# Kernel optimization log

Hardware: AMD Instinct MI355X
Metric: run time of the kernel (lower is better)

## Reference

```python
import jax, jax.numpy as jnp
import numpy as np
from jax import lax

V, D, B, L, T, H, C = 100000, 128, 512, 20, 20, 32, 33
N, E = B * L, B * (L - 1)
SCALE = 12.0

def _l2n(x, eps=1e-12):
    return x / (jnp.linalg.norm(x, axis=-1, keepdims=True) + eps)

def setup_inputs():
    key = jax.random.key(0)
    ks = jax.random.split(key, 30)
    stdv = 1.0 / np.sqrt(D)
    u = lambda k, s: jax.random.uniform(k, s, jnp.float32, -stdv, stdv)
    params = dict(
        emb=u(ks[0], (V, D)),
        W1=u(ks[1], (D, D)), W2=u(ks[2], (D, D)),
        gru_wih=u(ks[3], (3 * D, 2 * D)), gru_whh=u(ks[4], (3 * D, D)),
        gru_bih=u(ks[5], (3 * D,)), gru_bhh=u(ks[6], (3 * D,)),
        fcu_w=u(ks[7], (D, D)), fcv_w=u(ks[8], (D, D)), fcv_b=u(ks[9], (D,)),
        fce_w=u(ks[10], (D,)), fcsr_w=u(ks[11], (D, 2 * D)),
        red_w=u(ks[12], (H, D)), red_b=u(ks[13], (H,)),
        rec_w=u(ks[14], (D, H)), rec_b=u(ks[15], (D,)),
        cde_w1=u(ks[16], (128, H)), cde_b1=u(ks[17], (128,)),
        cde_w2=u(ks[18], (C * H, 128)), cde_b2=u(ks[19], (C * H,)),
        init_w=u(ks[20], (H, C)), init_b=u(ks[21], (H,)),
    )
    nodes = jnp.arange(N).reshape(B, L)  # B session graphs, L nodes each
    params.update(
        w=jax.random.uniform(ks[22], (E,), jnp.float32, 0.1, 1.0),
        times=jnp.cumsum(jax.random.uniform(ks[23], (B, T), jnp.float32, 0.05, 1.0), axis=1),
        iid=jax.random.randint(ks[24], (N,), 0, V),
        src=nodes[:, :-1].reshape(-1),
        dst=nodes[:, 1:].reshape(-1),
        seg_ids=jnp.repeat(jnp.arange(B), L),
        last_nodes=nodes[:, -1],
        embeds_ids=jax.random.randint(ks[25], (B, T), 0, V),
    )
    return params

def reference(emb, W1, W2, gru_wih, gru_whh, gru_bih, gru_bhh, fcu_w, fcv_w, fcv_b,
              fce_w, fcsr_w, red_w, red_b, rec_w, rec_b, cde_w1, cde_b1, cde_w2,
              cde_b2, init_w, init_b, w, times, iid, src, dst, seg_ids, last_nodes,
              embeds_ids):
    feat = _l2n(emb[iid])  # [N,D]
    # --- SRGNN layer: edge-weighted mean message passing (both directions) + GRUCell ---
    def wmean(s, d):
        msum = jax.ops.segment_sum(feat[s] * w[:, None], d, num_segments=N)
        wsum = jax.ops.segment_sum(w, d, num_segments=N)[:, None]
        return jnp.where(wsum > 0, msum / jnp.where(wsum == 0, 1.0, wsum), 0.0)
    hn = jnp.concatenate([wmean(src, dst) @ W1.T, wmean(dst, src) @ W2.T], axis=1)
    gi = hn @ gru_wih.T + gru_bih
    gh = feat @ gru_whh.T + gru_bhh
    i_r, i_z, i_n = jnp.split(gi, 3, axis=1)
    h_r, h_z, h_n = jnp.split(gh, 3, axis=1)
    r = jax.nn.sigmoid(i_r + h_r)
    zg = jax.nn.sigmoid(i_z + h_z)
    ng = jnp.tanh(i_n + r * h_n)
    out = (1.0 - zg) * ng + zg * feat  # NOTE: computed but unused downstream, exactly as original
    # --- neural CDE over the session item sequence (linear interp knots at t=0..T-1, RK4 per knot) ---
    fode = _l2n(emb[embeds_ids] @ red_w.T + red_b)          # [B,T,H]
    X = jnp.concatenate([times[..., None], fode], axis=-1)  # [B,T,C]
    z0 = X[:, 0] @ init_w.T + init_b                        # [B,H]
    def fz(zt):
        h1 = jax.nn.relu(zt @ cde_w1.T + cde_b1)
        return jnp.tanh(h1 @ cde_w2.T + cde_b2).reshape(B, H, C)
    dX = jnp.swapaxes(X[:, 1:] - X[:, :-1], 0, 1)           # [T-1,B,C] piecewise-constant dX/dt
    def step(zt, dx):
        g = lambda zz: jnp.einsum('bhc,bc->bh', fz(zz), dx)
        k1 = g(zt); k2 = g(zt + 0.5 * k1); k3 = g(zt + 0.5 * k2); k4 = g(zt + k3)
        return zt + (k1 + 2.0 * k2 + 2.0 * k3 + k4) / 6.0, None
    zT, _ = lax.scan(step, z0, dX)
    time_embeds = zT @ rec_w.T + rec_b                      # [B,D]
    # --- attention readout over graph segments ---
    featn = feat / jnp.linalg.norm(feat, axis=-1, keepdims=True)  # no-eps renorm, as original
    fu = featn @ fcu_w.T
    fv = featn[last_nodes] @ fcv_w.T + fcv_b
    e = jax.nn.sigmoid(fu + fv[seg_ids]) @ fce_w            # [N]
    emax = jax.ops.segment_max(e, seg_ids, num_segments=B)
    ee = jnp.exp(e - emax[seg_ids])
    alpha = ee / jax.ops.segment_sum(ee, seg_ids, num_segments=B)[seg_ids]
    sr_g = jax.ops.segment_sum(featn * alpha[:, None], seg_ids, num_segments=B)
    sr_l = featn[last_nodes]
    sr = _l2n(jnp.concatenate([sr_l, sr_g], axis=1) @ fcsr_w.T + time_embeds)
    logits = sr @ _l2n(emb).T                               # [B,V]
    return jax.nn.log_softmax(SCALE * logits, axis=-1)
```

## Files before the change

### kernel.cpp

```cpp
#include <hip/hip_runtime.h>
#include <cstdint>

#define VN 100000
#define DD 128
#define BB 512
#define LL 20
#define TT 20
#define HH 32
#define CC 33
#define NC (HH*CC)

typedef unsigned int u32;

#define DEV static __device__ __forceinline__

DEV float tanh_fast(float x){ float e=__expf(2.f*x); return 1.f - 2.f/(e+1.f); }

DEV float rdlane(float v, int l){
  return __int_as_float(__builtin_amdgcn_readlane(__float_as_int(v), l));
}

__global__ __launch_bounds__(576) void k_cde(
    const float* __restrict__ emb, const int* __restrict__ eids,
    const float* __restrict__ times,
    const float* __restrict__ red_w, const float* __restrict__ red_b,
    const float* __restrict__ w1, const float* __restrict__ b1,
    const float* __restrict__ w2, const float* __restrict__ b2,
    const float* __restrict__ iw, const float* __restrict__ ib,
    const float* __restrict__ rw, const float* __restrict__ rb,
    float* __restrict__ te){
  __shared__ float s_u[40*DD + 32*129];
  __shared__ float s_X[2*TT*CC];
  __shared__ float s_b1[DD];
  __shared__ float s_h1[2*DD];
  __shared__ float s_z[64], s_zs[64], s_ks[64], s_kp[64], s_kt[64];
  __shared__ float s_dx[2*CC];
  const int t = threadIdx.x;
  const int b0 = blockIdx.x*2;
  const int lane = t & 63;
  float* s_er = s_u;
  float* s_rw = s_u + 40*DD;
  float* s_w1 = s_u;

  float w2a[DD], w2b[DD];
  float b2a, b2b;
  int hq=0, qq=0;
  if (t < 512){
    hq = t>>4; qq = t&15;
    const int n0 = hq*CC + 2*qq;
    const float4* r0=(const float4*)(w2+(size_t)n0*DD);
    const float4* r1=(const float4*)(w2+(size_t)(n0+1)*DD);
    #pragma unroll 32
    for(int j=0;j<32;j++){
      float4 a=r0[j];
      w2a[4*j]=a.x; w2a[4*j+1]=a.y; w2a[4*j+2]=a.z; w2a[4*j+3]=a.w;
    }
    #pragma unroll 32
    for(int j=0;j<32;j++){
      float4 bv=r1[j];
      w2b[4*j]=bv.x; w2b[4*j+1]=bv.y; w2b[4*j+2]=bv.z; w2b[4*j+3]=bv.w;
    }
    b2a=b2[n0]; b2b=b2[n0+1];
  } else {
    const int l=t-512; const int nt=(l&31)*CC+32;
    const float4* r0=(const float4*)(w2+(size_t)nt*DD);
    #pragma unroll 32
    for(int j=0;j<32;j++){
      float4 a=r0[j];
      w2a[4*j]=a.x; w2a[4*j+1]=a.y; w2a[4*j+2]=a.z; w2a[4*j+3]=a.w;
    }
    b2a=b2[nt]; b2b=0.f;
  }

  for (int i=t;i<HH*DD;i+=576){ int hh=i>>7, d=i&127; s_rw[hh*129+d]=red_w[i]; }
  if (t<40){ int g=t/TT, tt2=t%TT; s_X[(g*TT+tt2)*CC]=times[(b0+g)*TT+tt2]; }
  for (int p=t;p<40*DD;p+=576){ int r=p>>7, e=p&127;
      s_er[p]=emb[(size_t)eids[b0*TT + r]*DD + e]; }
  __syncthreads();
  for (int task=t; task<40*HH; task+=576){
    int r=task>>5, hh=task&31;
    const float* wr=s_rw+hh*129;
    const float* er=s_er+(size_t)r*DD;
    float acc=red_b[hh];
    #pragma unroll 16
    for(int e=0;e<DD;e++) acc += er[e]*wr[e];
    float ss=acc*acc;
    #pragma unroll
    for(int o=16;o>0;o>>=1) ss+=__shfl_xor(ss,o,32);
    s_X[r*CC+1+hh]=acc/(sqrtf(ss)+1e-12f);
  }
  __syncthreads();
  for (int i=t;i<DD*HH;i+=576){ int j=i>>5, hh=i&31; s_w1[j*33+hh]=w1[i]; }
  if (t<DD) s_b1[t]=b1[t];
  if (t<64){
    int g=t>>5, hh=t&31;
    float acc=ib[hh];
    const float* x0=s_X+(size_t)(g*TT)*CC;
    #pragma unroll
    for(int c=0;c<CC;c++) acc += x0[c]*iw[hh*CC+c];
    s_z[t]=acc; s_zs[t]=acc;
  }

  for (int step=0; step<TT-1; step++){
    __syncthreads();
    if (t<2*CC){ int g=t/CC, c=t-g*CC;
      s_dx[t]=s_X[(g*TT+step+1)*CC+c]-s_X[(g*TT+step)*CC+c]; }
    __syncthreads();
    float dx00=0.f,dx01=0.f,dx10=0.f,dx11=0.f,dxt=0.f;
    if (t<512){ int c0=2*qq;
      dx00=s_dx[c0]; dx01=s_dx[c0+1]; dx10=s_dx[CC+c0]; dx11=s_dx[CC+c0+1];
    } else { int l=t-512; dxt=s_dx[(l>>5)*CC+32]; }

    for (int s=0;s<4;s++){
      if (t<256){
        const int g=t>>7, j=t&127, gb=(t>>7)*32;
        float zsv=s_zs[lane];
        float acc=s_b1[j];
        const float* wj=s_w1+j*33;
        #pragma unroll 32
        for(int hh=0;hh<32;hh++) acc += rdlane(zsv, gb+hh)*wj[hh];
        s_h1[g*DD+j]=fmaxf(acc,0.f);
      }
      __syncthreads();
      float h00=s_h1[lane],    h01=s_h1[64+lane];
      float h10=s_h1[DD+lane], h11=s_h1[DD+64+lane];
      if (t<512){
        float a00=b2a, a10=b2b, a01=b2a, a11=b2b;
        #pragma unroll 64
        for(int j=0;j<64;j++){
          float s0=rdlane(h00,j), s1=rdlane(h10,j);
          a00+=s0*w2a[j]; a10+=s0*w2b[j];
          a01+=s1*w2a[j]; a11+=s1*w2b[j];
        }
        #pragma unroll 64
        for(int j=0;j<64;j++){
          float s0=rdlane(h01,j), s1=rdlane(h11,j);
          a00+=s0*w2a[64+j]; a10+=s0*w2b[64+j];
          a01+=s1*w2a[64+j]; a11+=s1*w2b[64+j];
        }
        float pk0=tanh_fast(a00)*dx00 + tanh_fast(a10)*dx01;
        float pk1=tanh_fast(a01)*dx10 + tanh_fast(a11)*dx11;
        #pragma unroll
        for(int o=8;o>0;o>>=1){
          pk0+=__shfl_xor(pk0,o,16);
          pk1+=__shfl_xor(pk1,o,16);
        }
        if (qq==0){ s_kp[hq]=pk0; s_kp[32+hq]=pk1; }
      } else {
        const int l=t-512, gq=l>>5, ht=l&31;
        float a0=0.f, a1=0.f;
        #pragma unroll 64
        for(int j=0;j<64;j++){
          a0+=rdlane(h00,j)*w2a[j];
          a1+=rdlane(h10,j)*w2a[j];
        }
        #pragma unroll 64
        for(int j=0;j<64;j++){
          a0+=rdlane(h01,j)*w2a[64+j];
          a1+=rdlane(h11,j)*w2a[64+j];
        }
        float av = b2a + (gq ? a1 : a0);
        s_kt[gq*32+ht]=tanh_fast(av)*dxt;
      }
      __syncthreads();
      if (t<64){
        float k=s_kp[t]+s_kt[t];
        float zv=s_z[t];
        if(s==0){ s_ks[t]=k;        s_zs[t]=zv+0.5f*k; }
        else if(s==1){ s_ks[t]+=2.f*k; s_zs[t]=zv+0.5f*k; }
        else if(s==2){ s_ks[t]+=2.f*k; s_zs[t]=zv+k; }
        else { float zn=zv+(s_ks[t]+k)*(1.f/6.f); s_z[t]=zn; s_zs[t]=zn; }
      }
      __syncthreads();
    }
  }
  if (t<256){
    const int g=t>>7, d=t&127;
    float acc=rb[d];
    const float* zz=s_z+g*HH;
    const float4* rv=(const float4*)(rw + (size_t)d*HH);
    #pragma unroll 8
    for(int jj=0;jj<8;jj++){
      float4 vv=rv[jj];
      acc += zz[4*jj]*vv.x + zz[4*jj+1]*vv.y + zz[4*jj+2]*vv.z + zz[4*jj+3]*vv.w;
    }
    te[(size_t)(b0+g)*DD+d]=acc;
  }
}

__global__ __launch_bounds__(128) void k_attn(
    const float* __restrict__ emb, const int* __restrict__ iid,
    const int* __restrict__ last_nodes,
    const float* __restrict__ fcu_w, const float* __restrict__ fcv_w,
    const float* __restrict__ fcv_b, const float* __restrict__ fce_w,
    const float* __restrict__ fcsr_w,
    const float* __restrict__ te, float* __restrict__ sr){
  __shared__ float s_fn[LL*DD];
  __shared__ float s_inv[LL];
  __shared__ float s_e[LL], s_alpha[LL], s_red[2], s_sg[DD], s_fl[DD];
  const int t=threadIdx.x, b=blockIdx.x;
  for(int p=t;p<LL*DD;p+=128){
    int r=p>>7, e=p&127;
    s_fn[p]=emb[(size_t)iid[b*LL+r]*DD+e];
  }
  __syncthreads();
  { int w=t>>6, lane=t&63;
    for(int r=w;r<LL;r+=2){
      float a=s_fn[r*DD+lane], c=s_fn[r*DD+lane+64];
      float s=a*a+c*c;
      #pragma unroll
      for(int o=32;o>0;o>>=1) s+=__shfl_xor(s,o,64);
      if(lane==0) s_inv[r]=1.f/sqrtf(s);
    }
  }
  __syncthreads();
  for(int p=t;p<LL*DD;p+=128) s_fn[p]*=s_inv[p>>7];
  __syncthreads();
  int lr=last_nodes[b]-b*LL; if(lr<0||lr>=LL) lr=LL-1;
  s_fl[t]=s_fn[lr*DD+t];
  __syncthreads();
  float fv;
  {
    float acc=fcv_b[t];
    const float* wv=fcv_w + t*DD;
    #pragma unroll 8
    for(int j=0;j<DD;j++) acc += s_fl[j]*wv[j];
    fv=acc;
  }
  const float fce=fce_w[t];
  const float* wu=fcu_w + t*DD;
  for(int n=0;n<LL;n++){
    float fu=0.f;
    #pragma unroll 8
    for(int j=0;j<DD;j++) fu += s_fn[n*DD+j]*wu[j];
    float sv = fce/(1.f+__expf(-(fu+fv)));
    #pragma unroll
    for(int o=32;o>0;o>>=1) sv += __shfl_xor(sv,o,64);
    if((t&63)==0) s_red[t>>6]=sv;
    __syncthreads();
    if(t==0) s_e[n]=s_red[0]+s_red[1];
    __syncthreads();
  }
  if(t<64){
    float ev=(t<LL)? s_e[t] : -1e30f;
    float m=ev;
    #pragma unroll
    for(int o=32;o>0;o>>=1) m=fmaxf(m,__shfl_xor(m,o,64));
    float ex=(t<LL)? __expf(ev-m):0.f;
    float ssum=ex;
    #pragma unroll
    for(int o=32;o>0;o>>=1) ssum+=__shfl_xor(ssum,o,64);
    if(t<LL) s_alpha[t]=ex/ssum;
  }
  __syncthreads();
  float sg=0.f;
  for(int n=0;n<LL;n++) sg += s_alpha[n]*s_fn[n*DD+t];
  s_sg[t]=sg;
  __syncthreads();
  float pre=te[(size_t)b*DD+t];
  const float* wsr=fcsr_w + t*2*DD;
  #pragma unroll 8
  for(int j=0;j<DD;j++) pre += s_fl[j]*wsr[j];
  #pragma unroll 8
  for(int j=0;j<DD;j++) pre += s_sg[j]*wsr[DD+j];
  float ss=pre*pre;
  #pragma unroll
  for(int o=32;o>0;o>>=1) ss+=__shfl_xor(ss,o,64);
  if((t&63)==0) s_red[t>>6]=ss;
  __syncthreads();
  float tot=s_red[0]+s_red[1];
  sr[(size_t)b*DD+t]=pre/(sqrtf(tot)+1e-12f);
}

__global__ __launch_bounds__(256) void k_logits(
    const float* __restrict__ emb, const float* __restrict__ srr,
    float* __restrict__ out){
  const int v=blockIdx.x*256+threadIdx.x;
  if(v>=VN) return;
  const int bstart=blockIdx.y*256;
  float er[DD];
  {
    const float4* ev=(const float4*)emb + (size_t)v*32;
    #pragma unroll
    for(int j=0;j<32;j++){
      float4 u=ev[j];
      er[j*4+0]=u.x; er[j*4+1]=u.y; er[j*4+2]=u.z; er[j*4+3]=u.w;
    }
  }
  float nrm=0.f;
  #pragma unroll
  for(int d=0;d<DD;d++) nrm += er[d]*er[d];
  const float rn=12.f/(sqrtf(nrm)+1e-12f);
  for(int b=bstart;b<bstart+256;b++){
    const float* s=srr+(size_t)b*DD;
    float acc=0.f;
    #pragma unroll
    for(int d=0;d<DD;d++) acc += er[d]*s[d];
    out[(size_t)b*VN+v]=acc*rn;
  }
}

__global__ __launch_bounds__(256) void k_lse(const float* __restrict__ out,
                                             float* __restrict__ lse){
  const int b=blockIdx.x, t=threadIdx.x;
  const float4* rp=(const float4*)(out + (size_t)b*VN);
  float m=-1e30f, s=0.f;
  for(int i=t;i<VN/4;i+=256){
    float4 x=rp[i];
    float mx=fmaxf(fmaxf(x.x,x.y),fmaxf(x.z,x.w));
    if(mx>m){ s=s*__expf(m-mx); m=mx; }
    s += __expf(x.x-m)+__expf(x.y-m)+__expf(x.z-m)+__expf(x.w-m);
  }
  __shared__ float sm[256], ssb[256];
  sm[t]=m; ssb[t]=s;
  __syncthreads();
  for(int o=128;o>0;o>>=1){
    if(t<o){
      float m1=sm[t], m2=sm[t+o], s1=ssb[t], s2=ssb[t+o];
      float mm=fmaxf(m1,m2);
      sm[t]=mm; ssb[t]=s1*__expf(m1-mm)+s2*__expf(m2-mm);
    }
    __syncthreads();
  }
  if(t==0) lse[b]=sm[0]+logf(ssb[0]);
}

__global__ __launch_bounds__(256) void k_sub(float* __restrict__ out,
                                             const float* __restrict__ lse){
  const size_t i=(size_t)blockIdx.x*256+threadIdx.x;
  const int b=(int)((i*4)/VN);
  const float l=lse[b];
  float4* p=(float4*)out;
  float4 x=p[i];
  x.x-=l; x.y-=l; x.z-=l; x.w-=l;
  p[i]=x;
}

extern "C" void kernel_launch(void* const* d_in, const int* in_sizes, int n_in,
                              void* d_out, int out_size, void* d_ws, size_t ws_size,
                              hipStream_t stream){
  const float* emb    = (const float*)d_in[0];
  const float* fcu_w  = (const float*)d_in[7];
  const float* fcv_w  = (const float*)d_in[8];
  const float* fcv_b  = (const float*)d_in[9];
  const float* fce_w  = (const float*)d_in[10];
  const float* fcsr_w = (const float*)d_in[11];
  const float* red_w  = (const float*)d_in[12];
  const float* red_b  = (const float*)d_in[13];
  const float* rec_w  = (const float*)d_in[14];
  const float* rec_b  = (const float*)d_in[15];
  const float* cde_w1 = (const float*)d_in[16];
  const float* cde_b1 = (const float*)d_in[17];
  const float* cde_w2 = (const float*)d_in[18];
  const float* cde_b2 = (const float*)d_in[19];
  const float* init_w = (const float*)d_in[20];
  const float* init_b = (const float*)d_in[21];
  const float* times  = (const float*)d_in[23];
  const int* iid    = (const int*)d_in[24];
  const int* last_nodes = (const int*)d_in[28];
  const int* embeds_ids = (const int*)d_in[29];
  float* out = (float*)d_out;

  float* ws  = (float*)d_ws;
  float* te  = ws;
  float* sr  = te + (size_t)BB*DD;
  float* lse = sr + (size_t)BB*DD;

  k_cde   <<<BB/2, 576, 0, stream>>>(emb, embeds_ids, times, red_w, red_b,
                                     cde_w1, cde_b1, cde_w2, cde_b2,
                                     init_w, init_b, rec_w, rec_b, te);
  k_attn  <<<BB, 128, 0, stream>>>(emb, iid, last_nodes, fcu_w, fcv_w, fcv_b,
                                   fce_w, fcsr_w, te, sr);
  k_logits<<<dim3((VN+255)/256, 2), 256, 0, stream>>>(emb, sr, out);
  k_lse   <<<BB, 256, 0, stream>>>(out, lse);
  k_sub   <<<(int)(((size_t)BB*VN/4+255)/256), 256, 0, stream>>>(out, lse);
}
```

Baseline: 2.831 ms.

## Restructure CDE kernel to 512 threads with streamed cde_w2 rows and wave-reduced tail

The CDE vector-field kernel drops from 576 to 512 threads. Each thread now keeps one cde_w2 row in registers and streams a second row from global/L2 with software prefetch, instead of holding two rows. The 33rd channel is no longer handled by a separate 64-thread group; it is computed through wave-wide shuffle reductions spread across all waves. One redundant barrier per step is removed and launch bounds request two blocks per CU, for both this kernel and the logits kernel. The aim is lower register pressure, higher occupancy and no extra wave, at the cost of re-reading half the weights from cache on every RK stage.

```diff
diff --git a/kernel.cpp b/kernel.cpp
--- a/kernel.cpp
+++ b/kernel.cpp
@@ -20,7 +20,7 @@
   return __int_as_float(__builtin_amdgcn_readlane(__float_as_int(v), l));
 }
 
-__global__ __launch_bounds__(576) void k_cde(
+__global__ __launch_bounds__(512, 2) void k_cde(
     const float* __restrict__ emb, const int* __restrict__ eids,
     const float* __restrict__ times,
     const float* __restrict__ red_w, const float* __restrict__ red_b,
@@ -38,59 +38,53 @@
   const int t = threadIdx.x;
   const int b0 = blockIdx.x*2;
   const int lane = t & 63;
+  const int wv = t >> 6;
+  const int h  = t >> 4;
+  const int q  = t & 15;
   float* s_er = s_u;
   float* s_rw = s_u + 40*DD;
   float* s_w1 = s_u;
 
-  float w2a[DD], w2b[DD];
-  float b2a, b2b;
-  int hq=0, qq=0;
-  if (t < 512){
-    hq = t>>4; qq = t&15;
-    const int n0 = hq*CC + 2*qq;
-    const float4* r0=(const float4*)(w2+(size_t)n0*DD);
-    const float4* r1=(const float4*)(w2+(size_t)(n0+1)*DD);
-    #pragma unroll 32
-    for(int j=0;j<32;j++){
-      float4 a=r0[j];
-      w2a[4*j]=a.x; w2a[4*j+1]=a.y; w2a[4*j+2]=a.z; w2a[4*j+3]=a.w;
-    }
-    #pragma unroll 32
-    for(int j=0;j<32;j++){
-      float4 bv=r1[j];
-      w2b[4*j]=bv.x; w2b[4*j+1]=bv.y; w2b[4*j+2]=bv.z; w2b[4*j+3]=bv.w;
-    }
-    b2a=b2[n0]; b2b=b2[n0+1];
-  } else {
-    const int l=t-512; const int nt=(l&31)*CC+32;
-    const float4* r0=(const float4*)(w2+(size_t)nt*DD);
-    #pragma unroll 32
-    for(int j=0;j<32;j++){
-      float4 a=r0[j];
-      w2a[4*j]=a.x; w2a[4*j+1]=a.y; w2a[4*j+2]=a.z; w2a[4*j+3]=a.w;
-    }
-    b2a=b2[nt]; b2b=0.f;
-  }
-
-  for (int i=t;i<HH*DD;i+=576){ int hh=i>>7, d=i&127; s_rw[hh*129+d]=red_w[i]; }
+  float w2c[DD];
+  {
+    const float4* rc4 = (const float4*)(w2 + (size_t)(h*CC+q)*DD);
+    #pragma unroll
+    for (int j4=0;j4<32;j4++){
+      float4 v = rc4[j4];
+      w2c[4*j4]=v.x; w2c[4*j4+1]=v.y; w2c[4*j4+2]=v.z; w2c[4*j4+3]=v.w;
+    }
+  }
+  const float b2c = b2[h*CC+q];
+  const float b2s = b2[h*CC+16+q];
+  const float* rs = w2 + (size_t)(h*CC+16+q)*DD;
+  float w2t[8], b2t[4];
+  #pragma unroll
+  for (int r=0;r<4;r++){
+    const float* tr = w2 + (size_t)((4*wv+r)*CC+32)*DD;
+    w2t[2*r]   = tr[lane];
+    w2t[2*r+1] = tr[64+lane];
+    b2t[r]     = b2[(4*wv+r)*CC+32];
+  }
+
+  for (int i=t;i<HH*DD;i+=512){ int hh=i>>7, d=i&127; s_rw[hh*129+d]=red_w[i]; }
   if (t<40){ int g=t/TT, tt2=t%TT; s_X[(g*TT+tt2)*CC]=times[(b0+g)*TT+tt2]; }
-  for (int p=t;p<40*DD;p+=576){ int r=p>>7, e=p&127;
-      s_er[p]=emb[(size_t)eids[b0*TT + r]*DD + e]; }
-  __syncthreads();
-  for (int task=t; task<40*HH; task+=576){
+  for (int pi=t;pi<40*DD;pi+=512){ int r=pi>>7, e=pi&127;
+      s_er[pi]=emb[(size_t)eids[b0*TT+r]*DD+e]; }
+  __syncthreads();
+  for (int task=t; task<40*HH; task+=512){
     int r=task>>5, hh=task&31;
     const float* wr=s_rw+hh*129;
     const float* er=s_er+(size_t)r*DD;
     float acc=red_b[hh];
     #pragma unroll 16
     for(int e=0;e<DD;e++) acc += er[e]*wr[e];
-    float ss=acc*acc;
-    #pragma unroll
-    for(int o=16;o>0;o>>=1) ss+=__shfl_xor(ss,o,32);
-    s_X[r*CC+1+hh]=acc/(sqrtf(ss)+1e-12f);
-  }
-  __syncthreads();
-  for (int i=t;i<DD*HH;i+=576){ int j=i>>5, hh=i&31; s_w1[j*33+hh]=w1[i]; }
+    float ssq=acc*acc;
+    #pragma unroll
+    for(int o=16;o>0;o>>=1) ssq+=__shfl_xor(ssq,o,32);
+    s_X[r*CC+1+hh]=acc/(sqrtf(ssq)+1e-12f);
+  }
+  __syncthreads();
+  for (int i=t;i<DD*HH;i+=512){ int j=i>>5, hh=i&31; s_w1[j*33+hh]=w1[i]; }
   if (t<DD) s_b1[t]=b1[t];
   if (t<64){
     int g=t>>5, hh=t&31;
@@ -100,67 +94,75 @@
     for(int c=0;c<CC;c++) acc += x0[c]*iw[hh*CC+c];
     s_z[t]=acc; s_zs[t]=acc;
   }
-
+  __syncthreads();
+
+  const float4* rs4=(const float4*)rs;
   for (int step=0; step<TT-1; step++){
-    __syncthreads();
     if (t<2*CC){ int g=t/CC, c=t-g*CC;
       s_dx[t]=s_X[(g*TT+step+1)*CC+c]-s_X[(g*TT+step)*CC+c]; }
-    __syncthreads();
-    float dx00=0.f,dx01=0.f,dx10=0.f,dx11=0.f,dxt=0.f;
-    if (t<512){ int c0=2*qq;
-      dx00=s_dx[c0]; dx01=s_dx[c0+1]; dx10=s_dx[CC+c0]; dx11=s_dx[CC+c0+1];
-    } else { int l=t-512; dxt=s_dx[(l>>5)*CC+32]; }
-
     for (int s=0;s<4;s++){
+      float4 c0=rs4[0], c1=rs4[1], c2=rs4[2], c3=rs4[3];
       if (t<256){
         const int g=t>>7, j=t&127, gb=(t>>7)*32;
         float zsv=s_zs[lane];
         float acc=s_b1[j];
         const float* wj=s_w1+j*33;
-        #pragma unroll 32
-        for(int hh=0;hh<32;hh++) acc += rdlane(zsv, gb+hh)*wj[hh];
+        #pragma unroll
+        for(int hh=0;hh<HH;hh++) acc += rdlane(zsv, gb+hh)*wj[hh];
         s_h1[g*DD+j]=fmaxf(acc,0.f);
       }
       __syncthreads();
-      float h00=s_h1[lane],    h01=s_h1[64+lane];
-      float h10=s_h1[DD+lane], h11=s_h1[DD+64+lane];
-      if (t<512){
-        float a00=b2a, a10=b2b, a01=b2a, a11=b2b;
-        #pragma unroll 64
-        for(int j=0;j<64;j++){
-          float s0=rdlane(h00,j), s1=rdlane(h10,j);
-          a00+=s0*w2a[j]; a10+=s0*w2b[j];
-          a01+=s1*w2a[j]; a11+=s1*w2b[j];
+      {
+        float h00=s_h1[lane],    h01=s_h1[64+lane];
+        float h10=s_h1[DD+lane], h11=s_h1[DD+64+lane];
+        float a00=b2c, a01=b2c, a10=b2s, a11=b2s;
+        #pragma unroll
+        for (int jc=0;jc<8;jc++){
+          float4 n0=c0,n1=c1,n2=c2,n3=c3;
+          if (jc<7){ n0=rs4[4*jc+4]; n1=rs4[4*jc+5]; n2=rs4[4*jc+6]; n3=rs4[4*jc+7]; }
+          float cf[16]={c0.x,c0.y,c0.z,c0.w, c1.x,c1.y,c1.z,c1.w,
+                        c2.x,c2.y,c2.z,c2.w, c3.x,c3.y,c3.z,c3.w};
+          #pragma unroll
+          for (int jj=0;jj<16;jj++){
+            const int j=jc*16+jj;
+            float s0 = (j<64)? rdlane(h00,j) : rdlane(h01,j-64);
+            float s1 = (j<64)? rdlane(h10,j) : rdlane(h11,j-64);
+            a00 += s0*w2c[j]; a01 += s1*w2c[j];
+            a10 += s0*cf[jj]; a11 += s1*cf[jj];
+          }
+          c0=n0; c1=n1; c2=n2; c3=n3;
         }
-        #pragma unroll 64
-        for(int j=0;j<64;j++){
-          float s0=rdlane(h01,j), s1=rdlane(h11,j);
-          a00+=s0*w2a[64+j]; a10+=s0*w2b[64+j];
-          a01+=s1*w2a[64+j]; a11+=s1*w2b[64+j];
+        float pk0 = tanh_fast(a00)*s_dx[q]    + tanh_fast(a10)*s_dx[16+q];
+        float pk1 = tanh_fast(a01)*s_dx[CC+q] + tanh_fast(a11)*s_dx[CC+16+q];
+        #pragma unroll
+        for (int o=8;o>0;o>>=1){ pk0+=__shfl_xor(pk0,o,16); pk1+=__shfl_xor(pk1,o,16); }
+        if (q==0){ s_kp[h]=pk0; s_kp[32+h]=pk1; }
+        float p0=w2t[0]*h00+w2t[1]*h01;
+        float p1=w2t[0]*h10+w2t[1]*h11;
+        float p2=w2t[2]*h00+w2t[3]*h01;
+        float p3=w2t[2]*h10+w2t[3]*h11;
+        float p4=w2t[4]*h00+w2t[5]*h01;
+        float p5=w2t[4]*h10+w2t[5]*h11;
+        float p6=w2t[6]*h00+w2t[7]*h01;
+        float p7=w2t[6]*h10+w2t[7]*h11;
+        #pragma unroll
+        for (int o=1;o<64;o<<=1){
+          p0+=__shfl_xor(p0,o,64); p1+=__shfl_xor(p1,o,64);
+          p2+=__shfl_xor(p2,o,64); p3+=__shfl_xor(p3,o,64);
+          p4+=__shfl_xor(p4,o,64); p5+=__shfl_xor(p5,o,64);
+          p6+=__shfl_xor(p6,o,64); p7+=__shfl_xor(p7,o,64);
         }
-        float pk0=tanh_fast(a00)*dx00 + tanh_fast(a10)*dx01;
-        float pk1=tanh_fast(a01)*dx10 + tanh_fast(a11)*dx11;
-        #pragma unroll
-        for(int o=8;o>0;o>>=1){
-          pk0+=__shfl_xor(pk0,o,16);
-          pk1+=__shfl_xor(pk1,o,16);
+        if (lane==0){
+          float dt0=s_dx[32], dt1=s_dx[CC+32];
+          s_kt[4*wv+0]   =tanh_fast(p0+b2t[0])*dt0;
+          s_kt[32+4*wv+0]=tanh_fast(p1+b2t[0])*dt1;
+          s_kt[4*wv+1]   =tanh_fast(p2+b2t[1])*dt0;
+          s_kt[32+4*wv+1]=tanh_fast(p3+b2t[1])*dt1;
+          s_kt[4*wv+2]   =tanh_fast(p4+b2t[2])*dt0;
+          s_kt[32+4*wv+2]=tanh_fast(p5+b2t[2])*dt1;
+          s_kt[4*wv+3]   =tanh_fast(p6+b2t[3])*dt0;
+          s_kt[32+4*wv+3]=tanh_fast(p7+b2t[3])*dt1;
         }
-        if (qq==0){ s_kp[hq]=pk0; s_kp[32+hq]=pk1; }
-      } else {
-        const int l=t-512, gq=l>>5, ht=l&31;
-        float a0=0.f, a1=0.f;
-        #pragma unroll 64
-        for(int j=0;j<64;j++){
-          a0+=rdlane(h00,j)*w2a[j];
-          a1+=rdlane(h10,j)*w2a[j];
-        }
-        #pragma unroll 64
-        for(int j=0;j<64;j++){
-          a0+=rdlane(h01,j)*w2a[64+j];
-          a1+=rdlane(h11,j)*w2a[64+j];
-        }
-        float av = b2a + (gq ? a1 : a0);
-        s_kt[gq*32+ht]=tanh_fast(av)*dxt;
       }
       __syncthreads();
       if (t<64){
@@ -179,7 +181,7 @@
     float acc=rb[d];
     const float* zz=s_z+g*HH;
     const float4* rv=(const float4*)(rw + (size_t)d*HH);
-    #pragma unroll 8
+    #pragma unroll
     for(int jj=0;jj<8;jj++){
       float4 vv=rv[jj];
       acc += zz[4*jj]*vv.x + zz[4*jj+1]*vv.y + zz[4*jj+2]*vv.z + zz[4*jj+3]*vv.w;
@@ -272,7 +274,7 @@
   sr[(size_t)b*DD+t]=pre/(sqrtf(tot)+1e-12f);
 }
 
-__global__ __launch_bounds__(256) void k_logits(
+__global__ __launch_bounds__(256, 2) void k_logits(
     const float* __restrict__ emb, const float* __restrict__ srr,
     float* __restrict__ out){
   const int v=blockIdx.x*256+threadIdx.x;
@@ -366,7 +368,7 @@
   float* sr  = te + (size_t)BB*DD;
   float* lse = sr + (size_t)BB*DD;
 
-  k_cde   <<<BB/2, 576, 0, stream>>>(emb, embeds_ids, times, red_w, red_b,
+  k_cde   <<<BB/2, 512, 0, stream>>>(emb, embeds_ids, times, red_w, red_b,
                                      cde_w1, cde_b1, cde_w2, cde_b2,
                                      init_w, init_b, rec_w, rec_b, te);
   k_attn  <<<BB, 128, 0, stream>>>(emb, iid, last_nodes, fcu_w, fcv_w, fcv_b,
```

New measurement: 3.304 ms. +16.7%, slower.
